# Performance work log

Measured on AMD Instinct MI355X. Metric: run time of the kernel, lower is better.

Reference implementation:

```python
import jax, jax.numpy as jnp
import numpy as np

N = 20000      # nodes per type
E = 320000     # edges per relation
F = 512        # raw feature dim
H = 4          # attention heads
C = 128        # hidden_channels per head
B = 64         # batch_size (num graphs)
HH = H * C
INNER = 64
NEG_SLOPE = 0.2


def _gatv2(x_src, x_dst, ei, Wl, Wr, att, b):
    """PyG GATv2Conv (concat=True, add_self_loops=True, neg_slope=0.2).
    x_src:[Ns,Fin] x_dst:[Nd,Fin'] ei:[2,E] Wl,Wr:[Fin,H*C] att:[H,C] b:[H*C].
    Returns [Nd, H*C]. Self-loop edges appended (inputs assumed loop-free)."""
    n_dst = x_dst.shape[0]
    loop = jnp.arange(min(x_src.shape[0], n_dst), dtype=ei.dtype)
    src = jnp.concatenate([ei[0], loop])
    dst = jnp.concatenate([ei[1], loop])
    xl = (x_src @ Wl).reshape(-1, H, C)   # source-side transform
    xr = (x_dst @ Wr).reshape(-1, H, C)   # target-side transform
    e = jax.nn.leaky_relu(xl[src] + xr[dst], NEG_SLOPE)   # [E',H,C]
    logit = jnp.einsum('ehc,hc->eh', e, att)               # [E',H]
    m = jax.ops.segment_max(logit, dst, num_segments=n_dst)
    m = jnp.where(jnp.isfinite(m), m, 0.0)
    p = jnp.exp(logit - m[dst])
    s = jax.ops.segment_sum(p, dst, num_segments=n_dst)
    alpha = p / jnp.maximum(s[dst], 1e-16)                 # per-dst softmax
    out = jax.ops.segment_sum(alpha[:, :, None] * xl[src], dst, num_segments=n_dst)
    return out.reshape(n_dst, HH) + b


def _layer(x_i, x_j, ei_ii, ei_jj, ei_ij, ei_ji, Wl, Wr, att, b):
    # relation order: 0:(x_i->x_i) 1:(x_j->x_j) 2:(x_i->x_j) 3:(x_j->x_i); HeteroConv aggr='sum'
    oi = _gatv2(x_i, x_i, ei_ii, Wl[0], Wr[0], att[0], b[0]) \
       + _gatv2(x_j, x_i, ei_ji, Wl[3], Wr[3], att[3], b[3])
    oj = _gatv2(x_j, x_j, ei_jj, Wl[1], Wr[1], att[1], b[1]) \
       + _gatv2(x_i, x_j, ei_ij, Wl[2], Wr[2], att[2], b[2])
    # head-sum + tanh: x.view(-1, heads, hidden).sum(1).tanh()
    oi = jnp.tanh(oi.reshape(-1, H, C).sum(axis=1))
    oj = jnp.tanh(oj.reshape(-1, H, C).sum(axis=1))
    return oi, oj


def setup_inputs() -> dict:
    key = jax.random.key(0)
    ks = jax.random.split(key, 24)
    inp = {
        'x_i': jax.random.normal(ks[0], (N, F), jnp.float32),
        'x_j': jax.random.normal(ks[1], (N, F), jnp.float32),
        'ei_ii': jax.random.randint(ks[2], (2, E), 0, N, jnp.int32),
        'ei_jj': jax.random.randint(ks[3], (2, E), 0, N, jnp.int32),
        'ei_ij': jax.random.randint(ks[4], (2, E), 0, N, jnp.int32),
        'ei_ji': jax.random.randint(ks[5], (2, E), 0, N, jnp.int32),
        'batch_i': jnp.sort(jax.random.randint(ks[6], (N,), 0, B, jnp.int32)),
        'batch_j': jnp.sort(jax.random.randint(ks[7], (N,), 0, B, jnp.int32)),
        'Wl0': jax.random.normal(ks[8], (4, F, HH), jnp.float32) / np.sqrt(F),
        'Wr0': jax.random.normal(ks[9], (4, F, HH), jnp.float32) / np.sqrt(F),
        'att0': jax.random.normal(ks[10], (4, H, C), jnp.float32) / np.sqrt(C),
        'b0': jnp.zeros((4, HH), jnp.float32),
        'Wl1': jax.random.normal(ks[11], (4, C, HH), jnp.float32) / np.sqrt(C),
        'Wr1': jax.random.normal(ks[12], (4, C, HH), jnp.float32) / np.sqrt(C),
        'att1': jax.random.normal(ks[13], (4, H, C), jnp.float32) / np.sqrt(C),
        'b1': jnp.zeros((4, HH), jnp.float32),
        'W_out': jax.random.normal(ks[14], (C, 1), jnp.float32) / np.sqrt(C),
        'b_out': jnp.zeros((1,), jnp.float32),
        'W_i': jax.random.normal(ks[15], (C, INNER), jnp.float32) / np.sqrt(C),
        'b_i': jnp.zeros((INNER,), jnp.float32),
        'W_j': jax.random.normal(ks[16], (C, INNER), jnp.float32) / np.sqrt(C),
        'b_j': jnp.zeros((INNER,), jnp.float32),
    }
    return inp


def reference(x_i, x_j, ei_ii, ei_jj, ei_ij, ei_ji, batch_i, batch_j,
              Wl0, Wr0, att0, b0, Wl1, Wr1, att1, b1,
              W_out, b_out, W_i, b_i, W_j, b_j):
    x_i, x_j = _layer(x_i, x_j, ei_ii, ei_jj, ei_ij, ei_ji, Wl0, Wr0, att0, b0)
    x_i, x_j = _layer(x_i, x_j, ei_ii, ei_jj, ei_ij, ei_ji, Wl1, Wr1, att1, b1)
    # global_add_pool per graph, then unsqueeze(1) + tanh
    p_i = jnp.tanh(jax.ops.segment_sum(x_i, batch_i, num_segments=B))[:, None, :]  # [B,1,C]
    p_j = jnp.tanh(jax.ops.segment_sum(x_j, batch_j, num_segments=B))[:, None, :]
    y_i = p_i @ W_i + b_i   # [B,1,INNER]
    y_j = p_j @ W_j + b_j
    x = (p_i + p_j)[:, 0, :]            # cat along dim=1 then sum(dim=1)
    logits = jax.nn.sigmoid(x @ W_out + b_out)   # [B,1]
    return (logits, y_i, y_j)
```

## Files before the change

kernel.cpp:

```cpp
#include <hip/hip_runtime.h>

#define NN      20000
#define EE      320000
#define ETOT    340000
#define FD      512
#define HH_     4
#define CD      128
#define HHD     512
#define BG      64
#define INNERD  64

typedef __attribute__((ext_vector_type(8))) short bf16x8;
typedef __attribute__((ext_vector_type(4))) float f32x4;

__device__ __forceinline__ float bf2f(unsigned v) { return __uint_as_float(v << 16); }
__device__ __forceinline__ unsigned short f2bf(float f) {
    unsigned u = __float_as_uint(f);
    unsigned r = 0x7fffu + ((u >> 16) & 1u);
    return (unsigned short)((u + r) >> 16);
}
__device__ __forceinline__ void load8bf(const unsigned short* p, float* f) {
    uint4 u = *reinterpret_cast<const uint4*>(p);
    f[0] = bf2f(u.x & 0xffffu); f[1] = bf2f(u.x >> 16);
    f[2] = bf2f(u.y & 0xffffu); f[3] = bf2f(u.y >> 16);
// ... 424 lines not shown
            #pragma unroll
            for (int r = 0; r < 4; ++r) {
                int grow = tileM + wm + mi * 16 + quad * 4 + r;
                if (grow < M)
                    C[(size_t)grow * N + gcol] = f2bf(acc[mi][ni][r]);
            }
        }
    }
}

__global__ __launch_bounds__(256) void fused_aggr1(
    const int* __restrict__ rowptr, const unsigned short* __restrict__ srcs,
    const unsigned short* __restrict__ xl, const unsigned short* __restrict__ xr,
    const float* __restrict__ att,
    float* __restrict__ acc, int add_in, int fin_mode,
    const float* __restrict__ bA, const float* __restrict__ bB,
    unsigned short* __restrict__ z,
    const int* __restrict__ batch, float* __restrict__ pool)
{
    int dst = (int)((blockIdx.x * (size_t)blockDim.x + threadIdx.x) >> 6);
    int lane = threadIdx.x & 63;
    if (dst >= NN) return;
    int beg = rowptr[dst], end = rowptr[dst + 1];

    unsigned ub = *reinterpret_cast<const unsigned*>(xr + (size_t)dst * CD + lane * 2);
    float br0 = bf2f(ub & 0xffffu), br1 = bf2f(ub >> 16);
    float ta0 = att[lane * 2], ta1 = att[lane * 2 + 1];

    float n0 = 0.f, n1 = 0.f, den = 0.f;
    for (int k = beg; k < end; ++k) {
        int src = srcs[k];
        unsigned ua = *reinterpret_cast<const unsigned*>(xl + (size_t)src * CD + lane * 2);
        float a0 = bf2f(ua & 0xffffu), a1 = bf2f(ua >> 16);
        float v0 = a0 + br0, v1 = a1 + br1;
        v0 = (v0 > 0.f) ? v0 : 0.2f * v0;
        v1 = (v1 > 0.f) ? v1 : 0.2f * v1;
        float d = v0 * ta0 + v1 * ta1;
        #pragma unroll
        for (int off = 1; off < 64; off <<= 1)
            d += __shfl_xor(d, off);
        float p = expf(d);
        n0 += p * a0; n1 += p * a1; den += p;
    }
    float o0 = n0 / den, o1 = n1 / den;
    size_t ai = (size_t)dst * CD + lane * 2;
    if (add_in) { o0 += acc[ai]; o1 += acc[ai + 1]; }
    if (fin_mode == 0) {
        acc[ai] = o0; acc[ai + 1] = o1;
    } else {
        int c0 = lane * 2;
        float bb0 = 0.f, bb1 = 0.f;
        #pragma unroll
        for (int h = 0; h < HH_; ++h) {
            bb0 += bA[h * CD + c0]     + bB[h * CD + c0];
            bb1 += bA[h * CD + c0 + 1] + bB[h * CD + c0 + 1];
        }
        o0 = tanhf(o0 + bb0);
        o1 = tanhf(o1 + bb1);
        if (fin_mode == 1) {
            z[ai] = f2bf(o0); z[ai + 1] = f2bf(o1);
        } else {
            int b = batch[dst];
            atomicAdd(&pool[(size_t)b * CD + c0],     o0);
            atomicAdd(&pool[(size_t)b * CD + c0 + 1], o1);
        }
    }
}

__device__ __forceinline__ float edge_logit(const float* a, const float* br, const float* ta) {
    float d = 0.f;
    #pragma unroll
    for (int j = 0; j < 8; ++j) {
        float v = a[j] + br[j];
        v = fmaxf(v, 0.2f * v);
        d += v * ta[j];
    }
    return d;
}
__device__ __forceinline__ float quad_reduce(float d) {
    d += __shfl_xor(d, 1);
    d += __shfl_xor(d, 2);
    d += __shfl_xor(d, 4);
    d += __shfl_xor(d, 8);
    return d;
}
__device__ __forceinline__ void gat_drain(
    const unsigned short* __restrict__ sr, const unsigned short* __restrict__ xl,
    const float* br, const float* ta, int k, int e, float* n, float& den, int lane)
{
    for (; k + 2 <= e; k += 2) {
        int s0 = sr[k], s1 = sr[k + 1];
        float A0[8], A1[8];
        load8bf(xl + (size_t)s0 * HHD + lane * 8, A0);
        load8bf(xl + (size_t)s1 * HHD + lane * 8, A1);
        float d0 = quad_reduce(edge_logit(A0, br, ta));
        float d1 = quad_reduce(edge_logit(A1, br, ta));
        float p0 = __expf(d0), p1 = __expf(d1);
        den += p0;
        #pragma unroll
        for (int j = 0; j < 8; ++j) n[j] += p0 * A0[j];
        den += p1;
        #pragma unroll
        for (int j = 0; j < 8; ++j) n[j] += p1 * A1[j];
    }
    if (k < e) {
        int s0 = sr[k];
        float A0[8];
        load8bf(xl + (size_t)s0 * HHD + lane * 8, A0);
        float d0 = quad_reduce(edge_logit(A0, br, ta));
        float p0 = __expf(d0);
        den += p0;
        #pragma unroll
        for (int j = 0; j < 8; ++j) n[j] += p0 * A0[j];
    }
}

__device__ __forceinline__ void gat_rel(
    const int* __restrict__ rp, const unsigned short* __restrict__ sr,
    const unsigned short* __restrict__ xl, const unsigned short* __restrict__ xr,
    const float* __restrict__ att, int dst, int lane, float* o)
{
    int beg = rp[dst], end = rp[dst + 1];
    float br[8], ta[8];
    load8bf(xr + (size_t)dst * HHD + lane * 8, br);
    #pragma unroll
    for (int j = 0; j < 8; ++j) ta[j] = att[lane * 8 + j];
    float n[8] = {}; float den = 0.f;
    gat_drain(sr, xl, br, ta, beg, end, n, den, lane);
    float inv = 1.f / den;
    #pragma unroll
    for (int j = 0; j < 8; ++j) {
        o[j] = n[j] * inv;
        o[j] += __shfl_xor(o[j], 16);
        o[j] += __shfl_xor(o[j], 32);
    }
}

__device__ __forceinline__ void gat_rel2(
    const int* __restrict__ rp0, const unsigned short* __restrict__ sr0,
    const unsigned short* __restrict__ xl0, const unsigned short* __restrict__ xr0,
    const float* __restrict__ attA,
    const int* __restrict__ rp1, const unsigned short* __restrict__ sr1,
    const unsigned short* __restrict__ xl1, const unsigned short* __restrict__ xr1,
    const float* __restrict__ attB,
    int dst, int lane, float* o0, float* o1)
{
    int k0 = rp0[dst], e0 = rp0[dst + 1];
    int k1 = rp1[dst], e1 = rp1[dst + 1];
    float br0[8], br1[8], ta0[8], ta1[8];
    load8bf(xr0 + (size_t)dst * HHD + lane * 8, br0);
    load8bf(xr1 + (size_t)dst * HHD + lane * 8, br1);
    #pragma unroll
    for (int j = 0; j < 8; ++j) { ta0[j] = attA[lane * 8 + j]; ta1[j] = attB[lane * 8 + j]; }

    float n0[8] = {}, n1[8] = {};
    float den0 = 0.f, den1 = 0.f;

    while (k0 + 2 <= e0 && k1 + 2 <= e1) {
        int sa0 = sr0[k0], sa1 = sr0[k0 + 1];
        int sb0 = sr1[k1], sb1 = sr1[k1 + 1];
        float A0[8], A1[8], B0[8], B1[8];
        load8bf(xl0 + (size_t)sa0 * HHD + lane * 8, A0);
        load8bf(xl0 + (size_t)sa1 * HHD + lane * 8, A1);
        load8bf(xl1 + (size_t)sb0 * HHD + lane * 8, B0);
        load8bf(xl1 + (size_t)sb1 * HHD + lane * 8, B1);
        float dA0 = quad_reduce(edge_logit(A0, br0, ta0));
        float dA1 = quad_reduce(edge_logit(A1, br0, ta0));
        float dB0 = quad_reduce(edge_logit(B0, br1, ta1));
        float dB1 = quad_reduce(edge_logit(B1, br1, ta1));
        float pA0 = __expf(dA0), pA1 = __expf(dA1);
        float pB0 = __expf(dB0), pB1 = __expf(dB1);
        den0 += pA0;
        #pragma unroll
        for (int j = 0; j < 8; ++j) n0[j] += pA0 * A0[j];
        den0 += pA1;
        #pragma unroll
        for (int j = 0; j < 8; ++j) n0[j] += pA1 * A1[j];
        den1 += pB0;
        #pragma unroll
        for (int j = 0; j < 8; ++j) n1[j] += pB0 * B0[j];
        den1 += pB1;
        #pragma unroll
        for (int j = 0; j < 8; ++j) n1[j] += pB1 * B1[j];
        k0 += 2; k1 += 2;
    }
    gat_drain(sr0, xl0, br0, ta0, k0, e0, n0, den0, lane);
    gat_drain(sr1, xl1, br1, ta1, k1, e1, n1, den1, lane);

    float i0 = 1.f / den0, i1 = 1.f / den1;
    #pragma unroll
    for (int j = 0; j < 8; ++j) {
        o0[j] = n0[j] * i0;
        o0[j] += __shfl_xor(o0[j], 16);
        o0[j] += __shfl_xor(o0[j], 32);
        o1[j] = n1[j] * i1;
        o1[j] += __shfl_xor(o1[j], 16);
        o1[j] += __shfl_xor(o1[j], 32);
    }
}

__device__ __forceinline__ void aggr4d_body(
    int dst, int lane,
    const int* __restrict__ rp0, const unsigned short* __restrict__ sr0,
    const unsigned short* __restrict__ xl0, const unsigned short* __restrict__ xr0,
    const float* __restrict__ attA,
    const int* __restrict__ rp1, const unsigned short* __restrict__ sr1,
    const unsigned short* __restrict__ xl1, const unsigned short* __restrict__ xr1,
    const float* __restrict__ attB,
    float* __restrict__ acc, int fin_mode,
    const float* __restrict__ bA, const float* __restrict__ bB,
    unsigned short* __restrict__ z)
{
    float o0[8], o1[8];
    gat_rel2(rp0, sr0, xl0, xr0, attA, rp1, sr1, xl1, xr1, attB, dst, lane, o0, o1);
    #pragma unroll
    for (int j = 0; j < 8; ++j) o1[j] += o0[j];

    if (lane < 16) {
        size_t ai = (size_t)dst * CD + lane * 8;
        int c0 = lane * 8;
        #pragma unroll
        for (int j = 0; j < 8; ++j) {
            float bb = 0.f;
            #pragma unroll
            for (int h = 0; h < HH_; ++h)
                bb += bA[h * CD + c0 + j] + bB[h * CD + c0 + j];
            o1[j] = tanhf(o1[j] + bb);
        }
        if (fin_mode == 1) {
            #pragma unroll
            for (int j = 0; j < 8; ++j) z[ai + j] = f2bf(o1[j]);
        } else {
            #pragma unroll
            for (int j = 0; j < 8; ++j) acc[ai + j] = o1[j];
        }
    }
}

__global__ __launch_bounds__(256) void fused_aggr4(
    const int* __restrict__ rowptr, const unsigned short* __restrict__ srcs,
    const unsigned short* __restrict__ xl, const unsigned short* __restrict__ xr,
    const float* __restrict__ att,
    float* __restrict__ acc, int add_in, int fin_mode,
    const float* __restrict__ bA, const float* __restrict__ bB,
    unsigned short* __restrict__ z,
    const int* __restrict__ batch, float* __restrict__ pool)
{
    int dst = (int)((blockIdx.x * (size_t)blockDim.x + threadIdx.x) >> 6);
    int lane = threadIdx.x & 63;
    if (dst >= NN) return;

    float o[8];
    gat_rel(rowptr, srcs, xl, xr, att, dst, lane, o);

    if (lane < 16) {
        size_t ai = (size_t)dst * CD + lane * 8;
        if (add_in) {
            #pragma unroll
            for (int j = 0; j < 8; ++j) o[j] += acc[ai + j];
        }
        if (fin_mode == 0) {
            #pragma unroll
            for (int j = 0; j < 8; ++j) acc[ai + j] = o[j];
        } else {
            int c0 = lane * 8;
            #pragma unroll
            for (int j = 0; j < 8; ++j) {
                float bb = 0.f;
                #pragma unroll
                for (int h = 0; h < HH_; ++h)
                    bb += bA[h * CD + c0 + j] + bB[h * CD + c0 + j];
                o[j] = tanhf(o[j] + bb);
            }
            if (fin_mode == 1) {
                #pragma unroll
                for (int j = 0; j < 8; ++j) z[ai + j] = f2bf(o[j]);
            } else {
                #pragma unroll
                for (int j = 0; j < 8; ++j) acc[ai + j] = o[j];
            }
        }
    }
}

__global__ __launch_bounds__(256) void fused_aggr4d(
    const int* __restrict__ rp0, const unsigned short* __restrict__ sr0,
    const unsigned short* __restrict__ xl0, const unsigned short* __restrict__ xr0,
    const float* __restrict__ attA,
    const int* __restrict__ rp1, const unsigned short* __restrict__ sr1,
    const unsigned short* __restrict__ xl1, const unsigned short* __restrict__ xr1,
    const float* __restrict__ attB,
    float* __restrict__ acc, int fin_mode,
    const float* __restrict__ bA, const float* __restrict__ bB,
    unsigned short* __restrict__ z,
    const int* __restrict__ batch, float* __restrict__ pool)
{
    int dst = (int)((blockIdx.x * (size_t)blockDim.x + threadIdx.x) >> 6);
    int lane = threadIdx.x & 63;
    if (dst >= NN) return;
    aggr4d_body(dst, lane, rp0, sr0, xl0, xr0, attA, rp1, sr1, xl1, xr1, attB,
                acc, fin_mode, bA, bB, z);
}

template <typename TA, bool A_EXACT>
__global__ __launch_bounds__(256, 3) void gemm_aggr_fused(
    int ngemm,
    const TA* __restrict__ A0, const TA* __restrict__ A1,
    const TA* __restrict__ A2, const TA* __restrict__ A3,
    const unsigned short* __restrict__ B0h, const unsigned short* __restrict__ B0l,
    const unsigned short* __restrict__ B1h, const unsigned short* __restrict__ B1l,
    const unsigned short* __restrict__ B2h, const unsigned short* __restrict__ B2l,
    const unsigned short* __restrict__ B3h, const unsigned short* __restrict__ B3l,
    unsigned short* __restrict__ C0, unsigned short* __restrict__ C1,
    unsigned short* __restrict__ C2, unsigned short* __restrict__ C3,
    int M, int K, int N,
    const int* __restrict__ rp0, const unsigned short* __restrict__ sr0,
    const unsigned short* __restrict__ xl0, const unsigned short* __restrict__ xr0,
    const float* __restrict__ attA,
    const int* __restrict__ rp1, const unsigned short* __restrict__ sr1,
    const unsigned short* __restrict__ xl1, const unsigned short* __restrict__ xr1,
    const float* __restrict__ attB,
    float* __restrict__ acc, int fin_mode,
    const float* __restrict__ bA, const float* __restrict__ bB,
    unsigned short* __restrict__ zout)
{
    if ((int)blockIdx.x < ngemm) {
        int b = blockIdx.x;
        int xcd = b & 7, q8 = ngemm >> 3, r8 = ngemm & 7;
        int work = (xcd < r8 ? xcd * (q8 + 1) : r8 * (q8 + 1) + (xcd - r8) * q8) + (b >> 3);
        const int gx = N / 128, gy = (M + 127) / 128;
        int bx = work % gx; int t2 = work / gx; int by = t2 % gy; int bz = t2 / gy;
        const TA* A = bz == 0 ? A0 : bz == 1 ? A1 : bz == 2 ? A2 : A3;
        const unsigned short* Bh = bz == 0 ? B0h : bz == 1 ? B1h : bz == 2 ? B2h : B3h;
        const unsigned short* Bl = bz == 0 ? B0l : bz == 1 ? B1l : bz == 2 ? B2l : B3l;
        unsigned short* C = bz == 0 ? C0 : bz == 1 ? C1 : bz == 2 ? C2 : C3;
        gemm_body<TA, A_EXACT>(A, Bh, Bl, C, bx, by, M, K, N);
    } else {
        int dst = (int)(((blockIdx.x - ngemm) * (size_t)blockDim.x + threadIdx.x) >> 6);
        int lane = threadIdx.x & 63;
        if (dst >= NN) return;
        aggr4d_body(dst, lane, rp0, sr0, xl0, xr0, attA, rp1, sr1, xl1, xr1, attB,
                    acc, fin_mode, bA, bB, zout);
    }
}

__global__ __launch_bounds__(512) void pool_reduce(
    const float* __restrict__ acc, const int* __restrict__ batch,
    float* __restrict__ pool)
{
    int b = blockIdx.x;
    int t = threadIdx.x & (CD - 1);
    int q = threadIdx.x >> 7;
    int lo, hi;
    { int l = 0, r = NN; while (l < r) { int m = (l + r) >> 1; if (batch[m] < b) l = m + 1; else r = m; } lo = l; }
    { int l = lo, r = NN; while (l < r) { int m = (l + r) >> 1; if (batch[m] <= b) l = m + 1; else r = m; } hi = l; }
    float s = 0.f;
    for (int nrow = lo + q; nrow < hi; nrow += 4)
        s += acc[(size_t)nrow * CD + t];
    __shared__ float red[4][CD];
    red[q][t] = s;
    __syncthreads();
    if (q == 0)
        pool[(size_t)b * CD + t] = red[0][t] + red[1][t] + red[2][t] + red[3][t];
}

__global__ __launch_bounds__(128) void head_kernel(
    const float* __restrict__ pool_i, const float* __restrict__ pool_j,
    const float* __restrict__ W_out, const float* __restrict__ b_out,
    const float* __restrict__ W_i, const float* __restrict__ b_i,
    const float* __restrict__ W_j, const float* __restrict__ b_j,
    float* __restrict__ out)
{
    int b = blockIdx.x;
    int t = threadIdx.x;
    __shared__ float pi[CD], pj[CD];
    pi[t] = tanhf(pool_i[(size_t)b * CD + t]);
    pj[t] = tanhf(pool_j[(size_t)b * CD + t]);
    __syncthreads();
    if (t < INNERD) {
        float a = b_i[t];
        for (int c = 0; c < CD; ++c) a += pi[c] * W_i[c * INNERD + t];
        out[BG + (size_t)b * INNERD + t] = a;
    } else {
        int k = t - INNERD;
        float a = b_j[k];
        for (int c = 0; c < CD; ++c) a += pj[c] * W_j[c * INNERD + k];
        out[BG + BG * INNERD + (size_t)b * INNERD + k] = a;
    }
    if (t == 0) {
        float a = b_out[0];
        for (int c = 0; c < CD; ++c) a += (pi[c] + pj[c]) * W_out[c];
        out[b] = 1.f / (1.f + expf(-a));
    }
}

struct Ws {
    unsigned short *xl, *xr, *xl2, *xr2, *xl3, *xr3, *xl4, *xr4, *z_i, *z_j;
    float* acc;
    int *rowptr[4];
    unsigned short *srcs[4];
    int *cnt, *cursor;
    float *pool_i, *pool_j;
    unsigned short *wt0l_h, *wt0l_l, *wt0r_h, *wt0r_l;
    unsigned short *wt1l_h, *wt1l_l, *wt1r_h, *wt1r_l;
};

static void build_csr(const int* ei, int* rowptr, unsigned short* srcs,
                      int* cnt, int* cursor, hipStream_t stream) {
    hipMemsetAsync(cnt, 0, NN * sizeof(int), stream);
    csr_hist<<<(EE + 255) / 256, 256, 0, stream>>>(ei, cnt);
    csr_scan<<<1, 1024, 0, stream>>>(cnt, rowptr, cursor);
    csr_scatter16<<<(ETOT + 255) / 256, 256, 0, stream>>>(ei, cursor, srcs);
}

template <typename TA, bool A_EXACT>
static void run_group_fat_m(const TA* srcA[2], const TA* dstA[2],
                            const int* rp[2], const unsigned short* sr[2],
                            const int rids[2], int K,
                            const unsigned short* WTl_h, const unsigned short* WTl_l,
                            const unsigned short* WTr_h, const unsigned short* WTr_l,
                            const float* att, const float* bias, int fin_mode,
                            unsigned short* zout, const int* batch, float* pool,
                            const Ws& w, hipStream_t stream)
{
    dim3 gg(HHD / 128, (NN + 127) / 128, 4);
    size_t off0 = (size_t)rids[0] * HHD * K;
    size_t off1 = (size_t)rids[1] * HHD * K;
    gemm_mfma_t4<TA, A_EXACT><<<gg, 256, 0, stream>>>(
        srcA[0], dstA[0], srcA[1], dstA[1],
        WTl_h + off0, WTl_l + off0, WTr_h + off0, WTr_l + off0,
        WTl_h + off1, WTl_l + off1, WTr_h + off1, WTr_l + off1,
        w.xl, w.xr, w.xl2, w.xr2, NN, K, HHD);
    fused_aggr4d<<<NN / 4, 256, 0, stream>>>(
        rp[0], sr[0], w.xl, w.xr, att + (size_t)rids[0] * HHD,
        rp[1], sr[1], w.xl2, w.xr2, att + (size_t)rids[1] * HHD,
        w.acc, fin_mode,
        bias + (size_t)rids[0] * HHD, bias + (size_t)rids[1] * HHD,
        zout, batch, pool);
}

template <typename TA, bool A_EXACT>
static void run_group_fat_t(const TA* srcA[2], const TA* dstA[2],
                            const int* rp[2], const unsigned short* sr[2],
                            const int rids[2], int K,
                            const unsigned short* WTl_h, const unsigned short* WTl_l,
                            const unsigned short* WTr_h, const unsigned short* WTr_l,
                            const float* att, const float* bias, int fin_mode,
                            unsigned short* zout, const int* batch, float* pool,
                            const Ws& w, hipStream_t stream)
{
    dim3 gg(HHD / 128, (NN + 127) / 128, 2);
    const int ablocks = NN / 4;
    for (int q = 0; q < 2; ++q) {
        int r = rids[q];
        size_t off = (size_t)r * HHD * K;
        gemm_mfma_t<TA, A_EXACT><<<gg, 256, 0, stream>>>(
            srcA[q], dstA[q],
            WTl_h + off, WTl_l + off, WTr_h + off, WTr_l + off,
            w.xl, w.xr, NN, K, HHD);
        int fm = (q == 1) ? fin_mode : 0;
        fused_aggr4<<<ablocks, 256, 0, stream>>>(
            rp[q], sr[q], w.xl, w.xr,
            att + (size_t)r * HHD,
            w.acc, q > 0 ? 1 : 0, fm,
            bias + (size_t)rids[0] * HHD, bias + (size_t)rids[1] * HHD,
            zout, batch, pool);
    }
}

template <typename TA, bool A_EXACT>
static void run_group_fat(const TA* srcA[2], const TA* dstA[2],
                          const int* rp[2], const unsigned short* sr[2],
                          const int rids[2], int K,
                          const float* Wl, const float* Wr, const float* att,
                          const float* bias, int fin_mode,
                          unsigned short* zout, const int* batch, float* pool,
                          const Ws& w, hipStream_t stream)
{
    dim3 gg(HHD / 64, (NN + 63) / 64, 2);
    const int ablocks = NN / 4;
    for (int q = 0; q < 2; ++q) {
        int r = rids[q];
        gemm_mfma<TA, A_EXACT><<<gg, 256, 0, stream>>>(
            srcA[q], dstA[q],
            Wl + (size_t)r * K * HHD, Wr + (size_t)r * K * HHD, HHD,
            w.xl, w.xr, NN, K, HHD);
        int fm = (q == 1) ? fin_mode : 0;
        fused_aggr4<<<ablocks, 256, 0, stream>>>(
            rp[q], sr[q], w.xl, w.xr,
            att + (size_t)r * HHD,
            w.acc, q > 0 ? 1 : 0, fm,
            bias + (size_t)rids[0] * HHD, bias + (size_t)rids[1] * HHD,
            zout, batch, pool);
    }
}

template <typename TA, bool A_EXACT>
static void run_group_thin(const TA* srcA[2], const TA* dstA[2],
                           const int* eis[2], const int rids[2], int K,
                           const float* Wl, const float* Wr, const float* att,
                           const float* bias, int fin_mode,
                           unsigned short* zout, const int* batch, float* pool,
                           const Ws& w, hipStream_t stream)
{
    dim3 gg(2, (NN + 63) / 64, 2);
    const int ablocks = NN / 4;
    for (int q = 0; q < 2; ++q) {
        int r = rids[q];
        build_csr(eis[q], w.rowptr[0], w.srcs[0], w.cnt, w.cursor, stream);
        for (int h = 0; h < HH_; ++h) {
            const float* WlS = Wl + (size_t)r * K * HHD + h * CD;
            const float* WrS = Wr + (size_t)r * K * HHD + h * CD;
            gemm_mfma<TA, A_EXACT><<<gg, 256, 0, stream>>>(
                srcA[q], dstA[q], WlS, WrS, HHD, w.xl, w.xr, NN, K, CD);
            int pass = q * HH_ + h;
            int fm = (pass == 2 * HH_ - 1) ? fin_mode : 0;
            fused_aggr1<<<ablocks, 256, 0, stream>>>(
                w.rowptr[0], w.srcs[0], w.xl, w.xr,
                att + (size_t)r * HHD + h * CD,
                w.acc, pass > 0 ? 1 : 0, fm,
                bias + (size_t)rids[0] * HHD, bias + (size_t)rids[1] * HHD,
                zout, batch, pool);
        }
    }
}

extern "C" void kernel_launch(void* const* d_in, const int* in_sizes, int n_in,
                              void* d_out, int out_size, void* d_ws, size_t ws_size,
                              hipStream_t stream)
{
    const float* x_i   = (const float*)d_in[0];
    const float* x_j   = (const float*)d_in[1];
    const int* ei_ii   = (const int*)d_in[2];
    const int* ei_jj   = (const int*)d_in[3];
    const int* ei_ij   = (const int*)d_in[4];
    const int* ei_ji   = (const int*)d_in[5];
    const int* batch_i = (const int*)d_in[6];
    const int* batch_j = (const int*)d_in[7];
    const float* Wl0   = (const float*)d_in[8];
    const float* Wr0   = (const float*)d_in[9];
    const float* att0  = (const float*)d_in[10];
    const float* b0    = (const float*)d_in[11];
    const float* Wl1   = (const float*)d_in[12];
    const float* Wr1   = (const float*)d_in[13];
    const float* att1  = (const float*)d_in[14];
    const float* b1    = (const float*)d_in[15];
    const float* W_out = (const float*)d_in[16];
    const float* b_out = (const float*)d_in[17];
    const float* W_i   = (const float*)d_in[18];
    const float* b_i   = (const float*)d_in[19];
    const float* W_j   = (const float*)d_in[20];
    const float* b_j   = (const float*)d_in[21];
    float* out = (float*)d_out;

    const size_t FAT2_BYTES = (size_t)NN * HHD * 2 * 2 + (size_t)NN * CD * 4
                            + (size_t)NN * CD * 2 * 2 + 4 * (size_t)ETOT * 2
                            + 4 * (size_t)(NN + 4) * 4 + 4 * (size_t)NN * 4 * 2
                            + (size_t)BG * CD * 4 * 2;
    const size_t FAT1_BYTES = (size_t)NN * HHD * 2 * 2 + (size_t)NN * CD * 4
                            + (size_t)NN * CD * 2 * 2 + (size_t)ETOT * 2
                            + (size_t)(NN + 4) * 4 + (size_t)NN * 4 * 2
                            + (size_t)BG * CD * 4 * 2;
    const size_t WT0_ONE = (size_t)4 * 512 * 512 * 2;
    const size_t WT1_ONE = (size_t)4 * 512 * 128 * 2;
    const size_t WT_BYTES = 4 * WT0_ONE + 4 * WT1_ONE;
    const size_t X2_BYTES = 2 * (size_t)NN * HHD * 2;

    const int ncsr = (ws_size >= FAT2_BYTES) ? 4 : 1;
    const bool fat = (ws_size >= FAT1_BYTES);
    const bool fat_t = (ws_size >= FAT2_BYTES + WT_BYTES);
    const bool fat_m = (ws_size >= FAT2_BYTES + WT_BYTES + X2_BYTES);
    const bool fat_f = (ws_size >= FAT2_BYTES + WT_BYTES + 3 * X2_BYTES);

    Ws w;
    char* p = (char*)d_ws;
    size_t xbytes = fat ? (size_t)NN * HHD * 2 : (size_t)NN * CD * 2;
    w.xl     = (unsigned short*)p; p += xbytes;
    w.xr     = (unsigned short*)p; p += xbytes;
    w.acc    = (float*)p;          p += (size_t)NN * CD * 4;
    w.z_i    = (unsigned short*)p; p += (size_t)NN * CD * 2;
    w.z_j    = (unsigned short*)p; p += (size_t)NN * CD * 2;
    {
        int* rowptr_all = (int*)p;            p += (size_t)ncsr * (NN + 4) * 4;
        unsigned short* srcs_all = (unsigned short*)p; p += (size_t)ncsr * ETOT * 2;
        for (int r = 0; r < 4; ++r) {
            int rr = (r < ncsr) ? r : 0;
            w.rowptr[r] = rowptr_all + (size_t)rr * (NN + 4);
            w.srcs[r]   = srcs_all + (size_t)rr * ETOT;
        }
    }
    w.cnt    = (int*)p;            p += (size_t)ncsr * NN * 4;
    w.cursor = (int*)p;            p += (size_t)ncsr * NN * 4;
    w.pool_i = (float*)p;          p += (size_t)BG * CD * 4;
    w.pool_j = (float*)p;          p += (size_t)BG * CD * 4;
    if (fat_t) {
        w.wt0l_h = (unsigned short*)p; p += WT0_ONE;
        w.wt0l_l = (unsigned short*)p; p += WT0_ONE;
        w.wt0r_h = (unsigned short*)p; p += WT0_ONE;
        w.wt0r_l = (unsigned short*)p; p += WT0_ONE;
        w.wt1l_h = (unsigned short*)p; p += WT1_ONE;
        w.wt1l_l = (unsigned short*)p; p += WT1_ONE;
        w.wt1r_h = (unsigned short*)p; p += WT1_ONE;
        w.wt1r_l = (unsigned short*)p; p += WT1_ONE;
    }
    if (fat_m) {
        w.xl2 = (unsigned short*)p; p += (size_t)NN * HHD * 2;
        w.xr2 = (unsigned short*)p; p += (size_t)NN * HHD * 2;
    }
    if (fat_f) {
        w.xl3 = (unsigned short*)p; p += (size_t)NN * HHD * 2;
        w.xr3 = (unsigned short*)p; p += (size_t)NN * HHD * 2;
        w.xl4 = (unsigned short*)p; p += (size_t)NN * HHD * 2;
        w.xr4 = (unsigned short*)p; p += (size_t)NN * HHD * 2;
    }

    hipMemsetAsync(w.pool_i, 0, (size_t)BG * CD * sizeof(float), stream);
    hipMemsetAsync(w.pool_j, 0, (size_t)BG * CD * sizeof(float), stream);

    const int* eis_all[4] = { ei_ii, ei_jj, ei_ij, ei_ji };
    const float* srcA0_i[2] = { x_i, x_j };  const float* dstA0_i[2] = { x_i, x_i };
    const float* srcA0_j[2] = { x_j, x_i };  const float* dstA0_j[2] = { x_j, x_j };
    const int rids_i[2] = { 0, 3 };
    const int rids_j[2] = { 1, 2 };
    const unsigned short* srcA1_i[2] = { w.z_i, w.z_j };
    const unsigned short* dstA1_i[2] = { w.z_i, w.z_i };
    const unsigned short* srcA1_j[2] = { w.z_j, w.z_i };
    const unsigned short* dstA1_j[2] = { w.z_j, w.z_j };

    if (fat_t) {
        hipMemsetAsync(w.cnt, 0, 4 * NN * sizeof(int), stream);
        csr_hist4<<<(4 * EE + 255) / 256, 256, 0, stream>>>(
            ei_ii, ei_jj, ei_ij, ei_ji, w.cnt);
        csr_scan4<<<4, 1024, 0, stream>>>(w.cnt, w.rowptr[0], w.cursor);
        csr_scatter4<<<(4 * ETOT + 255) / 256, 256, 0, stream>>>(
            ei_ii, ei_jj, ei_ij, ei_ji, w.cursor, w.srcs[0]);
        wsplit_t<<<4 * (FD / 64) * 8, 256, 0, stream>>>(Wl0, w.wt0l_h, w.wt0l_l, FD);
        wsplit_t<<<4 * (FD / 64) * 8, 256, 0, stream>>>(Wr0, w.wt0r_h, w.wt0r_l, FD);
        wsplit_t<<<4 * (CD / 64) * 8, 256, 0, stream>>>(Wl1, w.wt1l_h, w.wt1l_l, CD);
        wsplit_t<<<4 * (CD / 64) * 8, 256, 0, stream>>>(Wr1, w.wt1r_h, w.wt1r_l, CD);

        const int* rp_i[2] = { w.rowptr[0], w.rowptr[3] };
        const unsigned short* sr_i[2] = { w.srcs[0], w.srcs[3] };
        const int* rp_j[2] = { w.rowptr[1], w.rowptr[2] };
        const unsigned short* sr_j[2] = { w.srcs[1], w.srcs[2] };

        if (fat_f) {
            const size_t o0 = (size_t)0 * HHD * FD, o3 = (size_t)3 * HHD * FD;
            const size_t o1 = (size_t)1 * HHD * FD, o2 = (size_t)2 * HHD * FD;
            dim3 gg(HHD / 128, (NN + 127) / 128, 4);
            gemm_mfma_t4<float, false><<<gg, 256, 0, stream>>>(
                x_i, x_i, x_j, x_i,
                w.wt0l_h + o0, w.wt0l_l + o0, w.wt0r_h + o0, w.wt0r_l + o0,
                w.wt0l_h + o3, w.wt0l_l + o3, w.wt0r_h + o3, w.wt0r_l + o3,
                w.xl, w.xr, w.xl2, w.xr2, NN, FD, HHD);
            const int ngemm = (HHD / 128) * ((NN + 127) / 128) * 4;
            gemm_aggr_fused<float, false><<<ngemm + NN / 4, 256, 0, stream>>>(
                ngemm,
                x_j, x_j, x_i, x_j,
                w.wt0l_h + o1, w.wt0l_l + o1, w.wt0r_h + o1, w.wt0r_l + o1,
                w.wt0l_h + o2, w.wt0l_l + o2, w.wt0r_h + o2, w.wt0r_l + o2,
                w.xl3, w.xr3, w.xl4, w.xr4, NN, FD, HHD,
                w.rowptr[0], w.srcs[0], w.xl, w.xr, att0 + (size_t)0 * HHD,
                w.rowptr[3], w.srcs[3], w.xl2, w.xr2, att0 + (size_t)3 * HHD,
                w.acc, 1, b0 + (size_t)0 * HHD, b0 + (size_t)3 * HHD, w.z_i);
            fused_aggr4d<<<NN / 4, 256, 0, stream>>>(
                w.rowptr[1], w.srcs[1], w.xl3, w.xr3, att0 + (size_t)1 * HHD,
                w.rowptr[2], w.srcs[2], w.xl4, w.xr4, att0 + (size_t)2 * HHD,
                w.acc, 1, b0 + (size_t)1 * HHD, b0 + (size_t)2 * HHD,
                w.z_j, nullptr, nullptr);
            dim3 g8(HHD / 128, (NN + 127) / 128, 8);
            gemm_mfma_L1x8<<<g8, 256, 0, stream>>>(
                w.z_i, w.z_j, w.wt1l_h, w.wt1l_l, w.wt1r_h, w.wt1r_l,
                w.xl, w.xr, w.xl2, w.xr2, w.xl3, w.xr3, w.xl4, w.xr4,
                NN, CD, HHD);
            fused_aggr4d<<<NN / 4, 256, 0, stream>>>(
                w.rowptr[0], w.srcs[0], w.xl, w.xr, att1 + (size_t)0 * HHD,
                w.rowptr[3], w.srcs[3], w.xl2, w.xr2, att1 + (size_t)3 * HHD,
                w.acc, 2, b1 + (size_t)0 * HHD, b1 + (size_t)3 * HHD,
                nullptr, nullptr, nullptr);
            pool_reduce<<<BG, 512, 0, stream>>>(w.acc, batch_i, w.pool_i);
            fused_aggr4d<<<NN / 4, 256, 0, stream>>>(
                w.rowptr[1], w.srcs[1], w.xl3, w.xr3, att1 + (size_t)1 * HHD,
                w.rowptr[2], w.srcs[2], w.xl4, w.xr4, att1 + (size_t)2 * HHD,
                w.acc, 2, b1 + (size_t)1 * HHD, b1 + (size_t)2 * HHD,
                nullptr, nullptr, nullptr);
            pool_reduce<<<BG, 512, 0, stream>>>(w.acc, batch_j, w.pool_j);
        } else if (fat_m) {
            run_group_fat_m<float, false>(srcA0_i, dstA0_i, rp_i, sr_i, rids_i, FD,
                                          w.wt0l_h, w.wt0l_l, w.wt0r_h, w.wt0r_l,
                                          att0, b0, 1, w.z_i, nullptr, nullptr, w, stream);
            run_group_fat_m<float, false>(srcA0_j, dstA0_j, rp_j, sr_j, rids_j, FD,
                                          w.wt0l_h, w.wt0l_l, w.wt0r_h, w.wt0r_l,
                                          att0, b0, 1, w.z_j, nullptr, nullptr, w, stream);
            run_group_fat_m<unsigned short, true>(srcA1_i, dstA1_i, rp_i, sr_i, rids_i, CD,
                                                  w.wt1l_h, w.wt1l_l, w.wt1r_h, w.wt1r_l,
                                                  att1, b1, 2, nullptr, batch_i, w.pool_i, w, stream);
            pool_reduce<<<BG, 512, 0, stream>>>(w.acc, batch_i, w.pool_i);
            run_group_fat_m<unsigned short, true>(srcA1_j, dstA1_j, rp_j, sr_j, rids_j, CD,
                                                  w.wt1l_h, w.wt1l_l, w.wt1r_h, w.wt1r_l,
                                                  att1, b1, 2, nullptr, batch_j, w.pool_j, w, stream);
            pool_reduce<<<BG, 512, 0, stream>>>(w.acc, batch_j, w.pool_j);
        } else {
            run_group_fat_t<float, false>(srcA0_i, dstA0_i, rp_i, sr_i, rids_i, FD,
                                          w.wt0l_h, w.wt0l_l, w.wt0r_h, w.wt0r_l,
                                          att0, b0, 1, w.z_i, nullptr, nullptr, w, stream);
            run_group_fat_t<float, false>(srcA0_j, dstA0_j, rp_j, sr_j, rids_j, FD,
                                          w.wt0l_h, w.wt0l_l, w.wt0r_h, w.wt0r_l,
                                          att0, b0, 1, w.z_j, nullptr, nullptr, w, stream);
            run_group_fat_t<unsigned short, true>(srcA1_i, dstA1_i, rp_i, sr_i, rids_i, CD,
                                                  w.wt1l_h, w.wt1l_l, w.wt1r_h, w.wt1r_l,
                                                  att1, b1, 2, nullptr, batch_i, w.pool_i, w, stream);
            pool_reduce<<<BG, 512, 0, stream>>>(w.acc, batch_i, w.pool_i);
            run_group_fat_t<unsigned short, true>(srcA1_j, dstA1_j, rp_j, sr_j, rids_j, CD,
                                                  w.wt1l_h, w.wt1l_l, w.wt1r_h, w.wt1r_l,
                                                  att1, b1, 2, nullptr, batch_j, w.pool_j, w, stream);
            pool_reduce<<<BG, 512, 0, stream>>>(w.acc, batch_j, w.pool_j);
        }
    } else if (fat) {
        if (ncsr == 4) {
            for (int r = 0; r < 4; ++r)
                build_csr(eis_all[r], w.rowptr[r], w.srcs[r], w.cnt, w.cursor, stream);
            const int* rp_i[2] = { w.rowptr[0], w.rowptr[3] };
            const unsigned short* sr_i[2] = { w.srcs[0], w.srcs[3] };
            const int* rp_j[2] = { w.rowptr[1], w.rowptr[2] };
            const unsigned short* sr_j[2] = { w.srcs[1], w.srcs[2] };
            run_group_fat<float, false>(srcA0_i, dstA0_i, rp_i, sr_i, rids_i, FD,
                                        Wl0, Wr0, att0, b0, 1, w.z_i, nullptr, nullptr, w, stream);
            run_group_fat<float, false>(srcA0_j, dstA0_j, rp_j, sr_j, rids_j, FD,
                                        Wl0, Wr0, att0, b0, 1, w.z_j, nullptr, nullptr, w, stream);
            run_group_fat<unsigned short, true>(srcA1_i, dstA1_i, rp_i, sr_i, rids_i, CD,
                                                Wl1, Wr1, att1, b1, 2, nullptr, batch_i, w.pool_i, w, stream);
            pool_reduce<<<BG, 512, 0, stream>>>(w.acc, batch_i, w.pool_i);
            run_group_fat<unsigned short, true>(srcA1_j, dstA1_j, rp_j, sr_j, rids_j, CD,
                                                Wl1, Wr1, att1, b1, 2, nullptr, batch_j, w.pool_j, w, stream);
            pool_reduce<<<BG, 512, 0, stream>>>(w.acc, batch_j, w.pool_j);
        } else {
            for (int pass = 0; pass < 4; ++pass) {
                const int* rids = (pass & 1) ? rids_j : rids_i;
                for (int q = 0; q < 2; ++q) {
                    int r = rids[q];
                    build_csr(eis_all[r], w.rowptr[0], w.srcs[0], w.cnt, w.cursor, stream);
                    dim3 gg(HHD / 64, (NN + 63) / 64, 2);
                    if (pass < 2) {
                        const float* sa = (pass == 0) ? srcA0_i[q] : srcA0_j[q];
                        const float* da = (pass == 0) ? dstA0_i[q] : dstA0_j[q];
                        gemm_mfma<float, false><<<gg, 256, 0, stream>>>(
                            sa, da, Wl0 + (size_t)r * FD * HHD, Wr0 + (size_t)r * FD * HHD,
                            HHD, w.xl, w.xr, NN, FD, HHD);
                        fused_aggr4<<<NN / 4, 256, 0, stream>>>(
                            w.rowptr[0], w.srcs[0], w.xl, w.xr, att0 + (size_t)r * HHD,
                            w.acc, q, (q == 1) ? 1 : 0,
                            b0 + (size_t)rids[0] * HHD, b0 + (size_t)rids[1] * HHD,
                            (pass == 0) ? w.z_i : w.z_j, nullptr, nullptr);
                    } else {
                        const unsigned short* sa = (pass == 2) ? srcA1_i[q] : srcA1_j[q];
                        const unsigned short* da = (pass == 2) ? dstA1_i[q] : dstA1_j[q];
                        gemm_mfma<unsigned short, true><<<gg, 256, 0, stream>>>(
                            sa, da, Wl1 + (size_t)r * CD * HHD, Wr1 + (size_t)r * CD * HHD,
                            HHD, w.xl, w.xr, NN, CD, HHD);
                        fused_aggr4<<<NN / 4, 256, 0, stream>>>(
                            w.rowptr[0], w.srcs[0], w.xl, w.xr, att1 + (size_t)r * HHD,
                            w.acc, q, (q == 1) ? 2 : 0,
                            b1 + (size_t)rids[0] * HHD, b1 + (size_t)rids[1] * HHD,
                            nullptr, (pass == 2) ? batch_i : batch_j,
                            (pass == 2) ? w.pool_i : w.pool_j);
                    }
                }
                if (pass == 2)
                    pool_reduce<<<BG, 512, 0, stream>>>(w.acc, batch_i, w.pool_i);
                else if (pass == 3)
                    pool_reduce<<<BG, 512, 0, stream>>>(w.acc, batch_j, w.pool_j);
            }
        }
    } else {
        const int* eis_i[2] = { ei_ii, ei_ji };
        const int* eis_j[2] = { ei_jj, ei_ij };
        run_group_thin<float, false>(srcA0_i, dstA0_i, eis_i, rids_i, FD, Wl0, Wr0, att0, b0,
                                     1, w.z_i, nullptr, nullptr, w, stream);
        run_group_thin<float, false>(srcA0_j, dstA0_j, eis_j, rids_j, FD, Wl0, Wr0, att0, b0,
                                     1, w.z_j, nullptr, nullptr, w, stream);
        run_group_thin<unsigned short, true>(srcA1_i, dstA1_i, eis_i, rids_i, CD, Wl1, Wr1, att1, b1,
                                             2, nullptr, batch_i, w.pool_i, w, stream);
        run_group_thin<unsigned short, true>(srcA1_j, dstA1_j, eis_j, rids_j, CD, Wl1, Wr1, att1, b1,
                                             2, nullptr, batch_j, w.pool_j, w, stream);
    }

    head_kernel<<<BG, 128, 0, stream>>>(w.pool_i, w.pool_j, W_out, b_out,
                                        W_i, b_i, W_j, b_j, out);
}
```

Baseline: 1.310 ms.

## Fuse layer-2 GEMMs with aggregation and merge paired aggregation and pooling launches

Adds a new workspace tier that holds a second accumulator, so both node types' layer-2 aggregations can run in one launch (fused_aggr4d_pair) and both pooling reductions in one launch (pool_reduce2). The schedule is rearranged so the layer-2 projections from z_i are computed inside the gemm_aggr_fused kernel that does the j-side layer-1 aggregation, and the z_j projections follow as one 4-way GEMM. The aim is fewer kernel launches and fewer serialized phases, with more overlap between GEMM and aggregation work. It needs extra workspace memory and depends on intricate buffer reuse (xl, xr, xl2 and so on), which raises the risk of aliasing mistakes.

```diff
diff --git a/kernel.cpp b/kernel.cpp
--- a/kernel.cpp
+++ b/kernel.cpp
@@ -750,6 +750,39 @@
                 acc, fin_mode, bA, bB, z);
 }
 
+__global__ __launch_bounds__(256) void fused_aggr4d_pair(
+    const int* __restrict__ irp0, const unsigned short* __restrict__ isr0,
+    const unsigned short* __restrict__ ixl0, const unsigned short* __restrict__ ixr0,
+    const float* __restrict__ iattA,
+    const int* __restrict__ irp1, const unsigned short* __restrict__ isr1,
+    const unsigned short* __restrict__ ixl1, const unsigned short* __restrict__ ixr1,
+    const float* __restrict__ iattB,
+    float* __restrict__ accA,
+    const float* __restrict__ ibA, const float* __restrict__ ibB,
+    const int* __restrict__ jrp0, const unsigned short* __restrict__ jsr0,
+    const unsigned short* __restrict__ jxl0, const unsigned short* __restrict__ jxr0,
+    const float* __restrict__ jattA,
+    const int* __restrict__ jrp1, const unsigned short* __restrict__ jsr1,
+    const unsigned short* __restrict__ jxl1, const unsigned short* __restrict__ jxr1,
+    const float* __restrict__ jattB,
+    float* __restrict__ accB,
+    const float* __restrict__ jbA, const float* __restrict__ jbB)
+{
+    const int half = NN / 4;
+    int lane = threadIdx.x & 63;
+    if ((int)blockIdx.x < half) {
+        int dst = (int)((blockIdx.x * (size_t)blockDim.x + threadIdx.x) >> 6);
+        if (dst >= NN) return;
+        aggr4d_body(dst, lane, irp0, isr0, ixl0, ixr0, iattA,
+                    irp1, isr1, ixl1, ixr1, iattB, accA, 2, ibA, ibB, nullptr);
+    } else {
+        int dst = (int)(((blockIdx.x - half) * (size_t)blockDim.x + threadIdx.x) >> 6);
+        if (dst >= NN) return;
+        aggr4d_body(dst, lane, jrp0, jsr0, jxl0, jxr0, jattA,
+                    jrp1, jsr1, jxl1, jxr1, jattB, accB, 2, jbA, jbB, nullptr);
+    }
+}
+
 template <typename TA, bool A_EXACT>
 __global__ __launch_bounds__(256, 3) void gemm_aggr_fused(
     int ngemm,
@@ -812,6 +845,30 @@
         pool[(size_t)b * CD + t] = red[0][t] + red[1][t] + red[2][t] + red[3][t];
 }
 
+__global__ __launch_bounds__(512) void pool_reduce2(
+    const float* __restrict__ accA, const int* __restrict__ batchA, float* __restrict__ poolA,
+    const float* __restrict__ accB, const int* __restrict__ batchB, float* __restrict__ poolB)
+{
+    int g = blockIdx.x;
+    const float* acc = (g < BG) ? accA : accB;
+    const int* batch = (g < BG) ? batchA : batchB;
+    float* pool = (g < BG) ? poolA : poolB;
+    int b = (g < BG) ? g : g - BG;
+    int t = threadIdx.x & (CD - 1);
+    int q = threadIdx.x >> 7;
+    int lo, hi;
+    { int l = 0, r = NN; while (l < r) { int m = (l + r) >> 1; if (batch[m] < b) l = m + 1; else r = m; } lo = l; }
+    { int l = lo, r = NN; while (l < r) { int m = (l + r) >> 1; if (batch[m] <= b) l = m + 1; else r = m; } hi = l; }
+    float s = 0.f;
+    for (int nrow = lo + q; nrow < hi; nrow += 4)
+        s += acc[(size_t)nrow * CD + t];
+    __shared__ float red[4][CD];
+    red[q][t] = s;
+    __syncthreads();
+    if (q == 0)
+        pool[(size_t)b * CD + t] = red[0][t] + red[1][t] + red[2][t] + red[3][t];
+}
+
 __global__ __launch_bounds__(128) void head_kernel(
     const float* __restrict__ pool_i, const float* __restrict__ pool_j,
     const float* __restrict__ W_out, const float* __restrict__ b_out,
@@ -844,7 +901,7 @@
 
 struct Ws {
     unsigned short *xl, *xr, *xl2, *xr2, *xl3, *xr3, *xl4, *xr4, *z_i, *z_j;
-    float* acc;
+    float *acc, *acc2;
     int *rowptr[4];
     unsigned short *srcs[4];
     int *cnt, *cursor;
@@ -1013,12 +1070,14 @@
     const size_t WT1_ONE = (size_t)4 * 512 * 128 * 2;
     const size_t WT_BYTES = 4 * WT0_ONE + 4 * WT1_ONE;
     const size_t X2_BYTES = 2 * (size_t)NN * HHD * 2;
+    const size_t ACC2_BYTES = (size_t)NN * CD * 4;
 
     const int ncsr = (ws_size >= FAT2_BYTES) ? 4 : 1;
     const bool fat = (ws_size >= FAT1_BYTES);
     const bool fat_t = (ws_size >= FAT2_BYTES + WT_BYTES);
     const bool fat_m = (ws_size >= FAT2_BYTES + WT_BYTES + X2_BYTES);
     const bool fat_f = (ws_size >= FAT2_BYTES + WT_BYTES + 3 * X2_BYTES);
+    const bool fat_g = (ws_size >= FAT2_BYTES + WT_BYTES + 3 * X2_BYTES + ACC2_BYTES);
 
     Ws w;
     char* p = (char*)d_ws;
@@ -1061,6 +1120,9 @@
         w.xl4 = (unsigned short*)p; p += (size_t)NN * HHD * 2;
         w.xr4 = (unsigned short*)p; p += (size_t)NN * HHD * 2;
     }
+    if (fat_g) {
+        w.acc2 = (float*)p; p += ACC2_BYTES;
+    }
 
     hipMemsetAsync(w.pool_i, 0, (size_t)BG * CD * sizeof(float), stream);
     hipMemsetAsync(w.pool_j, 0, (size_t)BG * CD * sizeof(float), stream);
@@ -1092,7 +1154,51 @@
         const int* rp_j[2] = { w.rowptr[1], w.rowptr[2] };
         const unsigned short* sr_j[2] = { w.srcs[1], w.srcs[2] };
 
-        if (fat_f) {
+        if (fat_g) {
+            const size_t o0 = (size_t)0 * HHD * FD, o3 = (size_t)3 * HHD * FD;
+            const size_t o1 = (size_t)1 * HHD * FD, o2 = (size_t)2 * HHD * FD;
+            const size_t p0 = (size_t)0 * HHD * CD, p1 = (size_t)1 * HHD * CD;
+            const size_t p2 = (size_t)2 * HHD * CD, p3 = (size_t)3 * HHD * CD;
+            dim3 gg(HHD / 128, (NN + 127) / 128, 4);
+            gemm_mfma_t4<float, false><<<gg, 256, 0, stream>>>(
+                x_i, x_i, x_j, x_i,
+                w.wt0l_h + o0, w.wt0l_l + o0, w.wt0r_h + o0, w.wt0r_l + o0,
+                w.wt0l_h + o3, w.wt0l_l + o3, w.wt0r_h + o3, w.wt0r_l + o3,
+                w.xl, w.xr, w.xl2, w.xr2, NN, FD, HHD);
+            const int ngemm0 = (HHD / 128) * ((NN + 127) / 128) * 4;
+            gemm_aggr_fused<float, false><<<ngemm0 + NN / 4, 256, 0, stream>>>(
+                ngemm0,
+                x_j, x_j, x_i, x_j,
+                w.wt0l_h + o1, w.wt0l_l + o1, w.wt0r_h + o1, w.wt0r_l + o1,
+                w.wt0l_h + o2, w.wt0l_l + o2, w.wt0r_h + o2, w.wt0r_l + o2,
+                w.xl3, w.xr3, w.xl4, w.xr4, NN, FD, HHD,
+                w.rowptr[0], w.srcs[0], w.xl, w.xr, att0 + (size_t)0 * HHD,
+                w.rowptr[3], w.srcs[3], w.xl2, w.xr2, att0 + (size_t)3 * HHD,
+                w.acc, 1, b0 + (size_t)0 * HHD, b0 + (size_t)3 * HHD, w.z_i);
+            gemm_aggr_fused<unsigned short, true><<<ngemm0 + NN / 4, 256, 0, stream>>>(
+                ngemm0,
+                w.z_i, w.z_i, w.z_i, w.z_i,
+                w.wt1l_h + p0, w.wt1l_l + p0, w.wt1r_h + p0, w.wt1r_l + p0,
+                w.wt1r_h + p3, w.wt1r_l + p3, w.wt1l_h + p2, w.wt1l_l + p2,
+                w.xl, w.xr, w.xr2, w.xl2, NN, CD, HHD,
+                w.rowptr[1], w.srcs[1], w.xl3, w.xr3, att0 + (size_t)1 * HHD,
+                w.rowptr[2], w.srcs[2], w.xl4, w.xr4, att0 + (size_t)2 * HHD,
+                w.acc, 1, b0 + (size_t)1 * HHD, b0 + (size_t)2 * HHD, w.z_j);
+            gemm_mfma_t4<unsigned short, true><<<gg, 256, 0, stream>>>(
+                w.z_j, w.z_j, w.z_j, w.z_j,
+                w.wt1l_h + p3, w.wt1l_l + p3, w.wt1l_h + p1, w.wt1l_l + p1,
+                w.wt1r_h + p1, w.wt1r_l + p1, w.wt1r_h + p2, w.wt1r_l + p2,
+                w.xl4, w.xl3, w.xr3, w.xr4, NN, CD, HHD);
+            fused_aggr4d_pair<<<2 * (NN / 4), 256, 0, stream>>>(
+                w.rowptr[0], w.srcs[0], w.xl, w.xr, att1 + (size_t)0 * HHD,
+                w.rowptr[3], w.srcs[3], w.xl4, w.xr2, att1 + (size_t)3 * HHD,
+                w.acc, b1 + (size_t)0 * HHD, b1 + (size_t)3 * HHD,
+                w.rowptr[1], w.srcs[1], w.xl3, w.xr3, att1 + (size_t)1 * HHD,
+                w.rowptr[2], w.srcs[2], w.xl2, w.xr4, att1 + (size_t)2 * HHD,
+                w.acc2, b1 + (size_t)1 * HHD, b1 + (size_t)2 * HHD);
+            pool_reduce2<<<2 * BG, 512, 0, stream>>>(
+                w.acc, batch_i, w.pool_i, w.acc2, batch_j, w.pool_j);
+        } else if (fat_f) {
             const size_t o0 = (size_t)0 * HHD * FD, o3 = (size_t)3 * HHD * FD;
             const size_t o1 = (size_t)1 * HHD * FD, o2 = (size_t)2 * HHD * FD;
             dim3 gg(HHD / 128, (NN + 127) / 128, 4);
```

Result: faster. 1.237 ms (-5.6%).
